# Kernel tuning notes

Hardware: AMD Instinct MI355X
Metric: run time of the kernel (lower is better)

The kernel has to match this reference:

```python
import jax, jax.numpy as jnp
import numpy as np

EPS = 1e-05
DECAY = 0.99
K = 2048   # codebook_size
D = 256    # codebook_dim


def setup_inputs() -> dict:
    key = jax.random.key(0)
    k1, k2, k3 = jax.random.split(key, 3)
    hidden_states = jax.random.normal(k1, (16, 4096, D), dtype=jnp.float32)
    embed_sum = jax.random.normal(k2, (K, D), dtype=jnp.float32)
    cluster_usage = jax.random.uniform(k3, (K,), dtype=jnp.float32)
    return {"hidden_states": hidden_states, "embed_sum": embed_sum, "cluster_usage": cluster_usage}


def reference(hidden_states, embed_sum, cluster_usage):
    # embed property: embed_sum / clamp(cluster_usage, min=eps)
    embed = embed_sum / jnp.clip(cluster_usage, EPS, None)[:, None]  # [K, D]

    shape = hidden_states.shape
    flat = hidden_states.reshape(-1, shape[-1])  # [N, D]

    # quantize: cdist(p=2) + argmin. argmin over squared distances is identical
    # to argmin over euclidean distances, avoiding the sqrt.
    x2 = jnp.sum(flat * flat, axis=-1, keepdims=True)          # [N, 1]
    e2 = jnp.sum(embed * embed, axis=-1)[None, :]              # [1, K]
    d2 = x2 - 2.0 * (flat @ embed.T) + e2                      # [N, K]
    flat_ind = jnp.argmin(d2, axis=-1)                         # [N]

    embed_ind = flat_ind.reshape(shape[:-1])                   # [B, T]
    quantize = embed[flat_ind].reshape(shape)                  # [B, T, D]

    # training-path EMA accumulation (scatter_add -> segment_sum), functional form
    counts = jax.ops.segment_sum(jnp.ones_like(flat_ind, dtype=flat.dtype), flat_ind, num_segments=K)
    sums = jax.ops.segment_sum(flat, flat_ind, num_segments=K)  # [K, D]
    new_cluster_usage = cluster_usage * DECAY + counts * (1.0 - DECAY)
    new_embed_sum = embed_sum * DECAY + sums * (1.0 - DECAY)

    return quantize, embed_ind, new_cluster_usage, new_embed_sum
```

## Files before the change

kernel.cpp:

```cpp
#include <hip/hip_runtime.h>

#define EPSF 1e-5f
#define DECAYF 0.99f
#define KCODES 2048
#define DIM 256

typedef _Float16 f16;
typedef f16 f16x8 __attribute__((ext_vector_type(8)));
typedef float f32x4 __attribute__((ext_vector_type(4)));

#define MFMA16(A, B, C) __builtin_amdgcn_mfma_f32_16x16x32_f16(A, B, C, 0, 0, 0)

#define OFF_AH 0
#define OFF_AL 16384
#define OFF_BH 32768
#define OFF_BL 49152

__device__ __forceinline__ void gload_lds16(const void* g, void* l) {
    __builtin_amdgcn_global_load_lds(
        (const __attribute__((address_space(1))) void*)g,
        (__attribute__((address_space(3))) void*)l, 16, 0, 0);
}

__global__ __launch_bounds__(256) void split_prep_kernel(
    const float* __restrict__ x, f16* __restrict__ xh, f16* __restrict__ xl, int nsplit,
    const float* __restrict__ embed_sum, const float* __restrict__ usage,
    float* __restrict__ embed, f16* __restrict__ eh, f16* __restrict__ el,
    float* __restrict__ e2, unsigned* __restrict__ pmax, unsigned* __restrict__ pmin)
{
    if ((int)blockIdx.x < nsplit) {
        int i = blockIdx.x * 256 + threadIdx.x;
        f32x4 v0 = ((const f32x4*)x)[2 * i];
        f32x4 v1 = ((const f32x4*)x)[2 * i + 1];
        f16x8 h, l;
        float p = 0.f;
        #pragma unroll
        for (int t = 0; t < 4; ++t) {
            f16 h0 = (f16)v0[t]; h[t] = h0; l[t] = (f16)(v0[t] - (float)h0);
            f16 h1 = (f16)v1[t]; h[t + 4] = h1; l[t + 4] = (f16)(v1[t] - (float)h1);
            p += v0[t] * v0[t] + v1[t] * v1[t];
        }
        ((f16x8*)xh)[i] = h;
        ((f16x8*)xl)[i] = l;
        #pragma unroll
        for (int m = 1; m <= 16; m <<= 1) p += __shfl_xor(p, m, 64);
        float q = fmaxf(p, __shfl_xor(p, 32, 64));
        __shared__ float wmax[4];
        if ((threadIdx.x & 63) == 0) wmax[threadIdx.x >> 6] = q;
        __syncthreads();
        if (threadIdx.x == 0) {
            float bm = fmaxf(fmaxf(wmax[0], wmax[1]), fmaxf(wmax[2], wmax[3]));
            atomicMax(&pmax[blockIdx.x & 63], __float_as_uint(bm) | 0x80000000u);
        }
    } else {
        int k = blockIdx.x - nsplit;
        int d = threadIdx.x;
        float inv = 1.0f / fmaxf(usage[k], EPSF);
        float e = embed_sum[k * DIM + d] * inv;
        embed[k * DIM + d] = e;
        float ec = fminf(fmaxf(e, -65000.0f), 65000.0f);
        f16 h = (f16)ec;
        f16 l = (f16)(ec - (float)h);
        eh[k * DIM + d] = h;
        el[k * DIM + d] = l;
        float sq = e * e;
        #pragma unroll
        for (int off = 32; off > 0; off >>= 1) sq += __shfl_down(sq, off, 64);
        __shared__ float ws[4];
        if ((threadIdx.x & 63) == 0) ws[threadIdx.x >> 6] = sq;
        __syncthreads();
        if (threadIdx.x == 0) {
            float s = ws[0] + ws[1] + ws[2] + ws[3];
            e2[k] = s;
            atomicMax(&pmin[k & 63], ~__float_as_uint(-s));
        }
    }
}

__global__ __launch_bounds__(256) void compactA_kernel(
    const float* __restrict__ e2, const unsigned* __restrict__ pmax,
    const unsigned* __restrict__ pmin, float* __restrict__ ce2,
    int* __restrict__ cmap, int* __restrict__ meta)
{
    __shared__ int ps[256];
    __shared__ float sT;
    const int t = threadIdx.x;
    if (t < 64) {
        unsigned km = pmax[t], kn = pmin[t];
        #pragma unroll
        for (int m = 1; m <= 32; m <<= 1) {
            km = max(km, (unsigned)__shfl_xor((int)km, m, 64));
            kn = max(kn, (unsigned)__shfl_xor((int)kn, m, 64));
        }
        if (t == 0) {
            float mx = __uint_as_float(km & 0x7FFFFFFFu);
            float mn = -__uint_as_float(~kn);
            float T0 = 2.0f * sqrtf(mx) + sqrtf(mn);
            sT = T0 * T0 * 1.0002f + 1.0f;
        }
    }
    __syncthreads();
    const float T = sT;
    int flag[8], pre[8], s = 0;
    float ev[8];
    #pragma unroll
    for (int j = 0; j < 8; ++j) {
        ev[j] = e2[t * 8 + j];
        flag[j] = (ev[j] <= T) ? 1 : 0;
        pre[j] = s; s += flag[j];
    }
    ps[t] = s;
    __syncthreads();
    for (int off = 1; off < 256; off <<= 1) {
        int v = (t >= off) ? ps[t - off] : 0;
        __syncthreads();
        ps[t] += v;
        __syncthreads();
    }
    const int ex = (t > 0) ? ps[t - 1] : 0;
    const int kp = ps[255];
    #pragma unroll
    for (int j = 0; j < 8; ++j) {
        const int k = t * 8 + j;
        if (flag[j]) {
            const int p = ex + pre[j];
            ce2[p] = ev[j];
            cmap[p] = k;
        }
    }
    for (int j = t; j < KCODES; j += 256)
        if (j >= kp) { ce2[j] = 3.4e38f; cmap[j] = 0; }
    if (t == 0) { meta[0] = kp; meta[1] = (kp + 255) & ~255; }
}

__global__ __launch_bounds__(512, 2) void argmin_kernel(
    const f16* __restrict__ xh, const f16* __restrict__ xl,
    const f16* __restrict__ eh, const f16* __restrict__ el,
    const float* __restrict__ ce2, const int* __restrict__ cmap,
    const int* __restrict__ meta, int* __restrict__ flat_ind, int* __restrict__ cnt)
{
    __shared__ __align__(1024) char lds[2 * 65536 + 8192];
    float* e2s = (float*)(lds + 131072);

    const int ncc = meta[1] >> 5;
    const int tid  = threadIdx.x;
    const int w    = tid >> 6, lane = tid & 63;
    const int l15  = lane & 15, l4 = lane >> 4;
    const int wm   = w >> 1, wn = w & 1;
    const int row0 = blockIdx.x * 256;
    const int gsw  = (lane & 3) ^ ((lane >> 3) & 3);
    const int lq   = lane >> 2;
    const int rslot = (l4 ^ ((l15 >> 1) & 3)) * 16;

    f32x4 acc[4][8];
    float best[16];
    int   bidx[16];
    #pragma unroll
    for (int t = 0; t < 16; ++t) { best[t] = 3.4e38f; bidx[t] = 0; }

    auto stageA = [&](const f16* rowbase, int koff, char* unit) {
        #pragma unroll
        for (int q = 0; q < 2; ++q) {
            const int r = w * 32 + q * 16 + lq;
            gload_lds16(rowbase + (size_t)r * DIM + koff + gsw * 8,
                        unit + w * 2048 + q * 1024 + lane * 16);
        }
    };
    auto stageB = [&](int tileBase, int koff, char* unitH, char* unitL) {
        #pragma unroll
        for (int q = 0; q < 2; ++q) {
            const int r = w * 32 + q * 16 + lq;
            const int pr = cmap[tileBase + r];
            gload_lds16(eh + (size_t)pr * DIM + koff + gsw * 8,
                        unitH + w * 2048 + q * 1024 + lane * 16);
            gload_lds16(el + (size_t)pr * DIM + koff + gsw * 8,
                        unitL + w * 2048 + q * 1024 + lane * 16);
        }
    };

    ((f32x4*)e2s)[tid] = ((const f32x4*)ce2)[tid];
    stageA(xh + (size_t)row0 * DIM, 0, lds + OFF_AH);
    stageA(xl + (size_t)row0 * DIM, 0, lds + OFF_AL);
    stageB(0, 0, lds + OFF_BH, lds + OFF_BL);

    for (int cc = 0; cc < ncc; ++cc) {
        char* buf  = lds + (cc & 1) * 65536;
        char* nbuf = lds + ((cc + 1) & 1) * 65536;
        const int ct = cc >> 3, sd = cc & 7;
        const int nn = cc + 1;
        const int nct = nn >> 3, nsd = nn & 7;
        const bool more = (nn < ncc);

        if (sd == 0) {
            #pragma unroll
            for (int i = 0; i < 4; ++i)
                #pragma unroll
                for (int j = 0; j < 8; ++j)
                    acc[i][j] = (f32x4){0.f, 0.f, 0.f, 0.f};
        }

        asm volatile("s_waitcnt vmcnt(0)" ::: "memory");
        __builtin_amdgcn_s_barrier();
        __builtin_amdgcn_sched_barrier(0);

        if (more) {
            stageA(xh + (size_t)row0 * DIM, nsd * 32, nbuf + OFF_AH);
            stageA(xl + (size_t)row0 * DIM, nsd * 32, nbuf + OFF_AL);
            stageB(nct * 256, nsd * 32, nbuf + OFF_BH, nbuf + OFF_BL);
        }

        f16x8 ah[4], al[4], bh[8], bl[8];
        #pragma unroll
        for (int i = 0; i < 4; ++i)
            ah[i] = *(const f16x8*)(buf + OFF_AH + (wm * 64 + i * 16 + l15) * 64 + rslot);
        #pragma unroll
        for (int j = 0; j < 8; ++j)
            bh[j] = *(const f16x8*)(buf + OFF_BH + (wn * 128 + j * 16 + l15) * 64 + rslot);
        #pragma unroll
        for (int i = 0; i < 4; ++i)
            al[i] = *(const f16x8*)(buf + OFF_AL + (wm * 64 + i * 16 + l15) * 64 + rslot);

        #pragma unroll
        for (int i = 0; i < 4; ++i)
            #pragma unroll
            for (int j = 0; j < 8; ++j)
                acc[i][j] = MFMA16(ah[i], bh[j], acc[i][j]);
        #pragma unroll
        for (int i = 0; i < 4; ++i)
            #pragma unroll
            for (int j = 0; j < 8; ++j)
                acc[i][j] = MFMA16(al[i], bh[j], acc[i][j]);

        #pragma unroll
        for (int j = 0; j < 8; ++j)
            bl[j] = *(const f16x8*)(buf + OFF_BL + (wn * 128 + j * 16 + l15) * 64 + rslot);
        #pragma unroll
        for (int i = 0; i < 4; ++i)
            #pragma unroll
            for (int j = 0; j < 8; ++j)
                acc[i][j] = MFMA16(ah[i], bl[j], acc[i][j]);

        if (sd == 7) {
            const int cbase = ct * 256 + wn * 128;
            #pragma unroll
            for (int j = 0; j < 8; ++j) {
                const int col = cbase + j * 16 + l15;
                const float e2v = e2s[col];
                #pragma unroll
                for (int i = 0; i < 4; ++i)
                    #pragma unroll
                    for (int r = 0; r < 4; ++r) {
                        float m = fmaf(-2.0f, acc[i][j][r], e2v);
                        const int tt_ = i * 4 + r;
                        if (m < best[tt_]) { best[tt_] = m; bidx[tt_] = col; }
                    }
            }
        }
    }

    __syncthreads();
    float* rv = (float*)lds;
    int*   ri = (int*)(lds + 4096);
    #pragma unroll
    for (int tt_ = 0; tt_ < 16; ++tt_) {
        float v = best[tt_];
        int  ix = bidx[tt_];
        #pragma unroll
        for (int m = 1; m <= 8; m <<= 1) {
            float ov = __shfl_xor(v, m, 64);
            int  oix = __shfl_xor(ix, m, 64);
            if (ov < v || (ov == v && oix < ix)) { v = ov; ix = oix; }
        }
        if (l15 == 0) {
            const int rl = wm * 64 + (tt_ >> 2) * 16 + l4 * 4 + (tt_ & 3);
            rv[rl * 2 + wn] = v;
            ri[rl * 2 + wn] = ix;
        }
    }
    __syncthreads();
    if (tid < 256) {
        float v0 = rv[tid * 2], v1 = rv[tid * 2 + 1];
        int   i0 = ri[tid * 2], i1 = ri[tid * 2 + 1];
        int ibc = (v1 < v0 || (v1 == v0 && i1 < i0)) ? i1 : i0;
        int ib = cmap[ibc];
        flat_ind[row0 + tid] = ib;
        unsigned long long pending = ~0ULL;
        while (pending) {
            int leader = __ffsll((long long)pending) - 1;
            int lind = __shfl(ib, leader, 64);
            unsigned long long same = __ballot(ib == lind);
            if ((tid & 63) == leader) atomicAdd(&cnt[lind], (int)__popcll(same));
            pending &= ~same;
        }
    }
}

__global__ __launch_bounds__(256) void scan_kernel(
    const int* __restrict__ cnt, int* __restrict__ offs, int* __restrict__ cursor)
{
    __shared__ int ps[256];
    const int t = threadIdx.x;
    int pre[8], s = 0;
    #pragma unroll
    for (int j = 0; j < 8; ++j) { pre[j] = s; s += cnt[t * 8 + j]; }
    ps[t] = s;
    __syncthreads();
    for (int off = 1; off < 256; off <<= 1) {
        int v = (t >= off) ? ps[t - off] : 0;
        __syncthreads();
        ps[t] += v;
        __syncthreads();
    }
    int ex = (t > 0) ? ps[t - 1] : 0;
    #pragma unroll
    for (int j = 0; j < 8; ++j) {
        offs[t * 8 + j]   = ex + pre[j];
        cursor[t * 8 + j] = ex + pre[j];
    }
}

__global__ __launch_bounds__(256) void assign_kernel(
    const int* __restrict__ flat_ind, int* __restrict__ cursor,
    int* __restrict__ rowlist, int* __restrict__ codesorted)
{
    const int i    = blockIdx.x * 256 + threadIdx.x;
    const int lane = threadIdx.x & 63;
    const int ind  = flat_ind[i];
    int pos = 0;
    unsigned long long pending = ~0ULL;
    while (pending) {
        int leader = __ffsll((long long)pending) - 1;
        int lind = __shfl(ind, leader, 64);
        unsigned long long same = __ballot(ind == lind);
        if (ind == lind) {
            int base = 0;
            if (lane == leader) base = atomicAdd(&cursor[lind], (int)__popcll(same));
            base = __shfl(base, leader, 64);
            pos = base + (int)__popcll(same & ((1ULL << lane) - 1ULL));
        }
        pending &= ~same;
    }
    rowlist[pos] = i;
    codesorted[pos] = ind;
}

__global__ __launch_bounds__(256) void codesum_kernel(
    const float* __restrict__ x, const int* __restrict__ rowlist,
    const int* __restrict__ codesorted, float* __restrict__ sums)
{
    const int p0 = blockIdx.x * 64;
    __shared__ int rows[64], codes[64];
    if (threadIdx.x < 64) {
        rows[threadIdx.x]  = rowlist[p0 + threadIdx.x];
        codes[threadIdx.x] = codesorted[p0 + threadIdx.x];
    }
    __syncthreads();
    const int d = threadIdx.x;
    float acc = 0.f;
    int cur = codes[0];
    #pragma unroll 4
    for (int r = 0; r < 64; ++r) {
        const int c = codes[r];
        if (c != cur) {
            atomicAdd(&sums[(size_t)cur * DIM + d], acc);
            acc = 0.f; cur = c;
        }
        acc += x[(size_t)rows[r] * DIM + d];
    }
    atomicAdd(&sums[(size_t)cur * DIM + d], acc);
}

__global__ __launch_bounds__(256) void quant_final_kernel(
    const float* __restrict__ embed, const int* __restrict__ flat_ind,
    float* __restrict__ out_q, float* __restrict__ out_ind_f, int N, int nq,
    const float* __restrict__ embed_sum, const float* __restrict__ usage,
    const float* __restrict__ sums, const int* __restrict__ cnt,
    float* __restrict__ out_usage, float* __restrict__ out_es)
{
    if ((int)blockIdx.x < nq) {
        int i = blockIdx.x * 256 + threadIdx.x;
        int row = i >> 6, c4 = i & 63;
        int ind = flat_ind[row];
        ((f32x4*)out_q)[i] = ((const f32x4*)embed)[ind * 64 + c4];
        if (i < N) out_ind_f[i] = (float)flat_ind[i];
    } else {
        const int k = blockIdx.x - nq, d = threadIdx.x;
        out_es[k * DIM + d] = embed_sum[k * DIM + d] * DECAYF + sums[k * DIM + d] * (1.0f - DECAYF);
        if (d == 0)
            out_usage[k] = usage[k] * DECAYF + (float)cnt[k] * (1.0f - DECAYF);
    }
}

extern "C" void kernel_launch(void* const* d_in, const int* in_sizes, int n_in,
                              void* d_out, int out_size, void* d_ws, size_t ws_size,
                              hipStream_t stream)
{
    const float* hs        = (const float*)d_in[0];
    const float* embed_sum = (const float*)d_in[1];
    const float* usage     = (const float*)d_in[2];
    const int N = in_sizes[0] / DIM;

    float* ws_f      = (float*)d_ws;
    float* embed     = ws_f;
    float* e2        = embed + KCODES * DIM;
    float* sums      = e2 + KCODES;
    int*   cnt       = (int*)(sums + KCODES * DIM);
    unsigned* pmax   = (unsigned*)(cnt + KCODES);
    unsigned* pmin   = pmax + 64;
    f16*   eh        = (f16*)(pmin + 64);
    f16*   el        = eh + KCODES * DIM;
    float* ce2       = (float*)(el + KCODES * DIM);
    int*   cmap      = (int*)(ce2 + KCODES);
    int*   meta      = cmap + KCODES;
    int*   offs      = meta + 16;
    int*   cursor    = offs + KCODES;
    int*   rowlist   = cursor + KCODES;
    int*   codesorted= rowlist + N;
    int*   flat_ind  = codesorted + N;

    float* out_q     = (float*)d_out;
    float* out_ind   = out_q + (size_t)N * DIM;
    float* out_usage = out_ind + N;
    float* out_es    = out_usage + KCODES;

    f16* xh = (f16*)out_q;
    f16* xl = xh + (size_t)N * DIM;

    hipMemsetAsync(sums, 0, (size_t)(KCODES * DIM + KCODES + 128) * sizeof(float), stream);

    const int nsplit = N * DIM / 8 / 256;
    split_prep_kernel<<<nsplit + KCODES, 256, 0, stream>>>(
        hs, xh, xl, nsplit, embed_sum, usage, embed, eh, el, e2, pmax, pmin);
    compactA_kernel<<<1, 256, 0, stream>>>(e2, pmax, pmin, ce2, cmap, meta);
    argmin_kernel<<<N / 256, 512, 0, stream>>>(xh, xl, eh, el, ce2, cmap, meta,
                                               flat_ind, cnt);
    scan_kernel<<<1, 256, 0, stream>>>(cnt, offs, cursor);
    assign_kernel<<<N / 256, 256, 0, stream>>>(flat_ind, cursor, rowlist, codesorted);
    codesum_kernel<<<N / 64, 256, 0, stream>>>(hs, rowlist, codesorted, sums);
    const int nq = N * DIM / 4 / 256;
    quant_final_kernel<<<nq + KCODES, 256, 0, stream>>>(
        embed, flat_ind, out_q, out_ind, N, nq,
        embed_sum, usage, sums, cnt, out_usage, out_es);
}
```

Baseline: 279.6 us.

## Fuse codesum with quantize gather, fold zeroing into prep, reorder LDS reads

The large memset of sums and counts moves into extra blocks of the split/prep kernel, so only the small pmax/pmin region still needs a memset. The codebook-sum scatter now runs in the same launch as the quantize gather, and the EMA finalize becomes its own small kernel. In the argmin main loop, the ah and bh LDS fragment reads now come before the async global-to-LDS staging, with the al read deferred until after the first MFMA group. The aim is fewer serialized launches and better overlap of LDS reads with staging, at the cost of one more kernel launch for finalize.

```diff
diff --git a/kernel.cpp b/kernel.cpp
--- a/kernel.cpp
+++ b/kernel.cpp
@@ -26,7 +26,8 @@
     const float* __restrict__ x, f16* __restrict__ xh, f16* __restrict__ xl, int nsplit,
     const float* __restrict__ embed_sum, const float* __restrict__ usage,
     float* __restrict__ embed, f16* __restrict__ eh, f16* __restrict__ el,
-    float* __restrict__ e2, unsigned* __restrict__ pmax, unsigned* __restrict__ pmin)
+    float* __restrict__ e2, unsigned* __restrict__ pmax, unsigned* __restrict__ pmin,
+    float* __restrict__ sums, int* __restrict__ cnt)
 {
     if ((int)blockIdx.x < nsplit) {
         int i = blockIdx.x * 256 + threadIdx.x;
@@ -52,7 +53,7 @@
             float bm = fmaxf(fmaxf(wmax[0], wmax[1]), fmaxf(wmax[2], wmax[3]));
             atomicMax(&pmax[blockIdx.x & 63], __float_as_uint(bm) | 0x80000000u);
         }
-    } else {
+    } else if ((int)blockIdx.x < nsplit + KCODES) {
         int k = blockIdx.x - nsplit;
         int d = threadIdx.x;
         float inv = 1.0f / fmaxf(usage[k], EPSF);
@@ -74,6 +75,10 @@
             e2[k] = s;
             atomicMax(&pmin[k & 63], ~__float_as_uint(-s));
         }
+    } else {
+        int k = blockIdx.x - nsplit - KCODES;
+        sums[k * DIM + threadIdx.x] = 0.f;
+        if (threadIdx.x == 0) cnt[k] = 0;
     }
 }
 
@@ -203,28 +208,30 @@
         __builtin_amdgcn_s_barrier();
         __builtin_amdgcn_sched_barrier(0);
 
+        f16x8 ah[4], al[4], bh[8], bl[8];
+        #pragma unroll
+        for (int i = 0; i < 4; ++i)
+            ah[i] = *(const f16x8*)(buf + OFF_AH + (wm * 64 + i * 16 + l15) * 64 + rslot);
+        #pragma unroll
+        for (int j = 0; j < 8; ++j)
+            bh[j] = *(const f16x8*)(buf + OFF_BH + (wn * 128 + j * 16 + l15) * 64 + rslot);
+        __builtin_amdgcn_sched_barrier(0);
+
         if (more) {
             stageA(xh + (size_t)row0 * DIM, nsd * 32, nbuf + OFF_AH);
             stageA(xl + (size_t)row0 * DIM, nsd * 32, nbuf + OFF_AL);
             stageB(nct * 256, nsd * 32, nbuf + OFF_BH, nbuf + OFF_BL);
         }
 
-        f16x8 ah[4], al[4], bh[8], bl[8];
-        #pragma unroll
-        for (int i = 0; i < 4; ++i)
-            ah[i] = *(const f16x8*)(buf + OFF_AH + (wm * 64 + i * 16 + l15) * 64 + rslot);
-        #pragma unroll
-        for (int j = 0; j < 8; ++j)
-            bh[j] = *(const f16x8*)(buf + OFF_BH + (wn * 128 + j * 16 + l15) * 64 + rslot);
-        #pragma unroll
-        for (int i = 0; i < 4; ++i)
-            al[i] = *(const f16x8*)(buf + OFF_AL + (wm * 64 + i * 16 + l15) * 64 + rslot);
-
         #pragma unroll
         for (int i = 0; i < 4; ++i)
             #pragma unroll
             for (int j = 0; j < 8; ++j)
                 acc[i][j] = MFMA16(ah[i], bh[j], acc[i][j]);
+
+        #pragma unroll
+        for (int i = 0; i < 4; ++i)
+            al[i] = *(const f16x8*)(buf + OFF_AL + (wm * 64 + i * 16 + l15) * 64 + rslot);
         #pragma unroll
         for (int i = 0; i < 4; ++i)
             #pragma unroll
@@ -344,51 +351,51 @@
     codesorted[pos] = ind;
 }
 
-__global__ __launch_bounds__(256) void codesum_kernel(
+__global__ __launch_bounds__(256) void codesum_quant_kernel(
     const float* __restrict__ x, const int* __restrict__ rowlist,
-    const int* __restrict__ codesorted, float* __restrict__ sums)
-{
-    const int p0 = blockIdx.x * 64;
-    __shared__ int rows[64], codes[64];
-    if (threadIdx.x < 64) {
-        rows[threadIdx.x]  = rowlist[p0 + threadIdx.x];
-        codes[threadIdx.x] = codesorted[p0 + threadIdx.x];
-    }
-    __syncthreads();
-    const int d = threadIdx.x;
-    float acc = 0.f;
-    int cur = codes[0];
-    #pragma unroll 4
-    for (int r = 0; r < 64; ++r) {
-        const int c = codes[r];
-        if (c != cur) {
-            atomicAdd(&sums[(size_t)cur * DIM + d], acc);
-            acc = 0.f; cur = c;
-        }
-        acc += x[(size_t)rows[r] * DIM + d];
-    }
-    atomicAdd(&sums[(size_t)cur * DIM + d], acc);
-}
-
-__global__ __launch_bounds__(256) void quant_final_kernel(
+    const int* __restrict__ codesorted, float* __restrict__ sums, int nc,
     const float* __restrict__ embed, const int* __restrict__ flat_ind,
-    float* __restrict__ out_q, float* __restrict__ out_ind_f, int N, int nq,
-    const float* __restrict__ embed_sum, const float* __restrict__ usage,
-    const float* __restrict__ sums, const int* __restrict__ cnt,
-    float* __restrict__ out_usage, float* __restrict__ out_es)
-{
-    if ((int)blockIdx.x < nq) {
-        int i = blockIdx.x * 256 + threadIdx.x;
+    float* __restrict__ out_q, float* __restrict__ out_ind_f, int N)
+{
+    if ((int)blockIdx.x < nc) {
+        const int p0 = blockIdx.x * 64;
+        __shared__ int rows[64], codes[64];
+        if (threadIdx.x < 64) {
+            rows[threadIdx.x]  = rowlist[p0 + threadIdx.x];
+            codes[threadIdx.x] = codesorted[p0 + threadIdx.x];
+        }
+        __syncthreads();
+        const int d = threadIdx.x;
+        float acc = 0.f;
+        int cur = codes[0];
+        #pragma unroll 4
+        for (int r = 0; r < 64; ++r) {
+            const int c = codes[r];
+            if (c != cur) {
+                atomicAdd(&sums[(size_t)cur * DIM + d], acc);
+                acc = 0.f; cur = c;
+            }
+            acc += x[(size_t)rows[r] * DIM + d];
+        }
+        atomicAdd(&sums[(size_t)cur * DIM + d], acc);
+    } else {
+        int i = (blockIdx.x - nc) * 256 + threadIdx.x;
         int row = i >> 6, c4 = i & 63;
         int ind = flat_ind[row];
         ((f32x4*)out_q)[i] = ((const f32x4*)embed)[ind * 64 + c4];
         if (i < N) out_ind_f[i] = (float)flat_ind[i];
-    } else {
-        const int k = blockIdx.x - nq, d = threadIdx.x;
-        out_es[k * DIM + d] = embed_sum[k * DIM + d] * DECAYF + sums[k * DIM + d] * (1.0f - DECAYF);
-        if (d == 0)
-            out_usage[k] = usage[k] * DECAYF + (float)cnt[k] * (1.0f - DECAYF);
-    }
+    }
+}
+
+__global__ __launch_bounds__(256) void finalize_kernel(
+    const float* __restrict__ embed_sum, const float* __restrict__ usage,
+    const float* __restrict__ sums, const int* __restrict__ cnt,
+    float* __restrict__ out_usage, float* __restrict__ out_es)
+{
+    const int k = blockIdx.x, d = threadIdx.x;
+    out_es[k * DIM + d] = embed_sum[k * DIM + d] * DECAYF + sums[k * DIM + d] * (1.0f - DECAYF);
+    if (d == 0)
+        out_usage[k] = usage[k] * DECAYF + (float)cnt[k] * (1.0f - DECAYF);
 }
 
 extern "C" void kernel_launch(void* const* d_in, const int* in_sizes, int n_in,
@@ -426,19 +433,21 @@
     f16* xh = (f16*)out_q;
     f16* xl = xh + (size_t)N * DIM;
 
-    hipMemsetAsync(sums, 0, (size_t)(KCODES * DIM + KCODES + 128) * sizeof(float), stream);
+    hipMemsetAsync(pmax, 0, 128 * sizeof(unsigned), stream);
 
     const int nsplit = N * DIM / 8 / 256;
-    split_prep_kernel<<<nsplit + KCODES, 256, 0, stream>>>(
-        hs, xh, xl, nsplit, embed_sum, usage, embed, eh, el, e2, pmax, pmin);
+    split_prep_kernel<<<nsplit + 2 * KCODES, 256, 0, stream>>>(
+        hs, xh, xl, nsplit, embed_sum, usage, embed, eh, el, e2, pmax, pmin,
+        sums, cnt);
     compactA_kernel<<<1, 256, 0, stream>>>(e2, pmax, pmin, ce2, cmap, meta);
     argmin_kernel<<<N / 256, 512, 0, stream>>>(xh, xl, eh, el, ce2, cmap, meta,
                                                flat_ind, cnt);
     scan_kernel<<<1, 256, 0, stream>>>(cnt, offs, cursor);
     assign_kernel<<<N / 256, 256, 0, stream>>>(flat_ind, cursor, rowlist, codesorted);
-    codesum_kernel<<<N / 64, 256, 0, stream>>>(hs, rowlist, codesorted, sums);
+    const int nc = N / 64;
     const int nq = N * DIM / 4 / 256;
-    quant_final_kernel<<<nq + KCODES, 256, 0, stream>>>(
-        embed, flat_ind, out_q, out_ind, N, nq,
-        embed_sum, usage, sums, cnt, out_usage, out_es);
-}
+    codesum_quant_kernel<<<nc + nq, 256, 0, stream>>>(
+        hs, rowlist, codesorted, sums, nc, embed, flat_ind, out_q, out_ind, N);
+    finalize_kernel<<<KCODES, 256, 0, stream>>>(embed_sum, usage, sums, cnt,
+                                                out_usage, out_es);
+}
```

Result: faster. 267.5 us (-4.3%).
